# Kernel optimization log

Hardware: AMD Instinct MI355X
Metric: run time of the kernel (lower is better)

Reference implementation:

```python
import jax, jax.numpy as jnp
import numpy as np

N = 100000
E = 1600000
IN_C = 256
OUT_C = 128


def setup_inputs() -> dict:
    key = jax.random.key(0)
    ks = jax.random.split(key, 8)
    x = jax.random.normal(ks[0], (N, IN_C), dtype=jnp.float32)
    edge_index = jax.random.randint(ks[1], (2, E), 0, N, dtype=jnp.int64)
    # GCNConv params (weight + bias)
    W = jax.random.normal(ks[2], (IN_C, OUT_C), dtype=jnp.float32) / np.sqrt(IN_C)
    b = jnp.zeros((OUT_C,), dtype=jnp.float32)
    # residual Linear params
    Wr = jax.random.normal(ks[3], (IN_C, OUT_C), dtype=jnp.float32) / np.sqrt(IN_C)
    br = jnp.zeros((OUT_C,), dtype=jnp.float32)
    # LayerNorm params
    gamma = jnp.ones((OUT_C,), dtype=jnp.float32)
    beta = jnp.zeros((OUT_C,), dtype=jnp.float32)
    return {"x": x, "edge_index": edge_index, "W": W, "b": b,
            "Wr": Wr, "br": br, "gamma": gamma, "beta": beta}


def _gcn_conv(x, src, dst, W, b):
    # PyG GCNConv: add self-loops, symmetric degree normalization,
    # transform first (out < in), then gather-scale-scatter.
    n = x.shape[0]
    loops = jnp.arange(n, dtype=src.dtype)
    src = jnp.concatenate([src, loops])
    dst = jnp.concatenate([dst, loops])
    ones = jnp.ones_like(dst, dtype=x.dtype)
    deg = jax.ops.segment_sum(ones, dst, num_segments=n)  # [N]
    dinv = jnp.where(deg > 0, jax.lax.rsqrt(deg), 0.0)
    norm = dinv[src] * dinv[dst]                           # [E+N]
    h = x @ W                                              # [N, out]
    msg = h[src] * norm[:, None]                           # [E+N, out]
    agg = jax.ops.segment_sum(msg, dst, num_segments=n)    # [N, out]
    return agg + b


def _layer_norm(x, gamma, beta, eps=1e-5):
    mu = jnp.mean(x, axis=-1, keepdims=True)
    var = jnp.mean(jnp.square(x - mu), axis=-1, keepdims=True)
    return (x - mu) * jax.lax.rsqrt(var + eps) * gamma + beta


def reference(x, edge_index, W, b, Wr, br, gamma, beta):
    src, dst = edge_index[0], edge_index[1]
    res = x @ Wr + br
    h = _gcn_conv(x, src, dst, W, b)
    out = _layer_norm(h + res, gamma, beta)
    return jax.nn.relu(out)
```

## Files before the change

kernel.cpp:

```cpp
#include <hip/hip_runtime.h>

typedef __attribute__((ext_vector_type(8))) short bf16x8;
typedef __attribute__((ext_vector_type(4))) float f32x4;
typedef __attribute__((ext_vector_type(8))) unsigned short ushort8;
typedef __attribute__((ext_vector_type(4))) unsigned short ushort4v;

__device__ __forceinline__ unsigned short f2bf(float f) {
  unsigned int u = __float_as_uint(f);
  u = u + 0x7FFFu + ((u >> 16) & 1u);
  return (unsigned short)(u >> 16);
}
__device__ __forceinline__ float bflo(unsigned int u) { return __uint_as_float(u << 16); }
__device__ __forceinline__ float bfhi(unsigned int u) { return __uint_as_float(u & 0xFFFF0000u); }

#define GLOAD_LDS16(g, l)                                                            \
  __builtin_amdgcn_global_load_lds((const __attribute__((address_space(1))) void*)(g), \
                                   (__attribute__((address_space(3))) void*)(l), 16, 0, 0)

__global__ void k_pre(const float* __restrict__ W, const float* __restrict__ Wr,
                      unsigned short* __restrict__ Wb,
                      const int* __restrict__ dst, int* __restrict__ deg,
                      int* __restrict__ rank, int E) {
  if (blockIdx.x < 8) {
    int t = blockIdx.x * 256 + threadIdx.x;
    int col = t >> 3, g = t & 7;
    const float* Ws = (col < 128) ? (W + col) : (Wr + (col - 128));
#pragma unroll
    for (int kt = 0; kt < 4; ++kt) {
      ushort8 u;
#pragma unroll
      for (int j = 0; j < 8; ++j) u[j] = f2bf(Ws[(size_t)(kt * 64 + g * 8 + j) * 128]);
      *(ushort8*)&Wb[kt * 16384 + col * 64 + ((g ^ (col & 7)) * 8)] = u;
    }
    return;
  }
  int base = ((blockIdx.x - 8) * 256 + threadIdx.x) * 4;
  if (base + 3 < E) {
    int4 d = *(const int4*)(dst + base);
    int r0 = atomicAdd(&deg[d.x], 1);
    int r1 = atomicAdd(&deg[d.y], 1);
    int r2 = atomicAdd(&deg[d.z], 1);
    int r3 = atomicAdd(&deg[d.w], 1);
    *(int4*)(rank + base) = make_int4(r0, r1, r2, r3);
  } else {
    for (int e = base; e < E; ++e) rank[e] = atomicAdd(&deg[dst[e]], 1);
  }
}

__global__ void k_fill(const int* __restrict__ src, const int* __restrict__ dst,
                       const int* __restrict__ rank, int* __restrict__ ssrc, int E) {
  int base = (blockIdx.x * blockDim.x + threadIdx.x) * 4;
  if (base + 3 < E) {
    int4 d = *(const int4*)(dst + base);
    int4 r = *(const int4*)(rank + base);
    int4 s = *(const int4*)(src + base);
    if (r.x < 64) ssrc[(size_t)d.x * 64 + r.x] = s.x;
    if (r.y < 64) ssrc[(size_t)d.y * 64 + r.y] = s.y;
    if (r.z < 64) ssrc[(size_t)d.z * 64 + r.z] = s.z;
    if (r.w < 64) ssrc[(size_t)d.w * 64 + r.w] = s.w;
  } else {
    for (int e = base; e < E; ++e) {
      int r = rank[e];
      if (r < 64) ssrc[(size_t)dst[e] * 64 + r] = src[e];
    }
  }
}

__global__ __launch_bounds__(512) void k_gemm(
    const float* __restrict__ x, const unsigned short* __restrict__ Wb,
    const float* __restrict__ br, const int* __restrict__ deg,
    unsigned short* __restrict__ hs, float* res, int N)
{
  __shared__ unsigned short xt[128 * 64];
  __shared__ unsigned short wt[256 * 64];
  int tid = threadIdx.x;
  int lane = tid & 63, w = tid >> 6;
  int lo = lane & 15, hi = lane >> 4;
  int brow = blockIdx.x * 128;

  f32x4 acc[16];
#pragma unroll
  for (int c = 0; c < 16; ++c) acc[c] = (f32x4){0.f, 0.f, 0.f, 0.f};

  for (int kt = 0; kt < 4; ++kt) {
    int k0 = kt * 64;
    const unsigned short* gw = Wb + kt * 16384;
#pragma unroll
    for (int i = 0; i < 4; ++i) {
      int off = i * 4096 + tid * 8;
      GLOAD_LDS16(gw + off, &wt[off]);
    }
#pragma unroll
    for (int r = 0; r < 4; ++r) {
      int idx = tid + 512 * r;
      int row = idx >> 4, kq = idx & 15;
      int node = brow + row;
      float4 v = make_float4(0.f, 0.f, 0.f, 0.f);
      if (node < N) v = *(const float4*)(x + (size_t)node * 256 + k0 + kq * 4);
      ushort4v u;
      u[0] = f2bf(v.x); u[1] = f2bf(v.y); u[2] = f2bf(v.z); u[3] = f2bf(v.w);
      int g = kq >> 1, h = kq & 1;
      *(ushort4v*)(&xt[row * 64 + ((g ^ (row & 7)) * 8) + h * 4]) = u;
    }
    __syncthreads();
#pragma unroll
    for (int kk = 0; kk < 2; ++kk) {
      int row = w * 16 + lo;
      int gsel = kk * 4 + hi;
      bf16x8 a = *(const bf16x8*)(&xt[row * 64 + ((gsel ^ (row & 7)) * 8)]);
      int gsw = (gsel ^ (lo & 7)) * 8;
#pragma unroll
      for (int c = 0; c < 16; ++c) {
        bf16x8 b = *(const bf16x8*)(&wt[(c * 16 + lo) * 64 + gsw]);
        acc[c] = __builtin_amdgcn_mfma_f32_16x16x32_bf16(a, b, acc[c], 0, 0, 0);
      }
    }
    __syncthreads();
  }
  float di4[4];
#pragma unroll
  for (int rg = 0; rg < 4; ++rg) {
    int row = brow + w * 16 + hi * 4 + rg;
    di4[rg] = (row < N) ? rsqrtf((float)(deg[row] + 1)) : 0.f;
  }
#pragma unroll
  for (int c = 0; c < 16; ++c) {
    int colo = c * 16 + lo;
#pragma unroll
    for (int rg = 0; rg < 4; ++rg) {
      int row = brow + w * 16 + hi * 4 + rg;
      if (row < N) {
        float v = acc[c][rg];
        if (colo < 128) hs[(size_t)row * 128 + colo] = f2bf(v * di4[rg]);
        else            res[(size_t)row * 128 + (colo - 128)] = v + br[colo - 128];
      }
    }
  }
}

__global__ __launch_bounds__(256) void k_agg(
    const unsigned int* __restrict__ hsb, const float* resin,
    const int* __restrict__ deg, const int* __restrict__ ssrc,
    const float* __restrict__ bias, const float* __restrict__ gamma,
    const float* __restrict__ beta, float* out, int N)
{
  int node = blockIdx.x * 4 + (threadIdx.x >> 6);
  int lane = threadIdx.x & 63;
  if (node >= N) return;
  unsigned int su = hsb[(size_t)node * 64 + lane];
  float ax = bflo(su), ay = bfhi(su);
  int cnt = deg[node];
  float di = rsqrtf((float)(cnt + 1));
  if (cnt > 64) cnt = 64;
  const int* sp = ssrc + (size_t)node * 64;
  int e = 0;
  for (; e + 16 <= cnt; e += 16) {
    int idx[16];
#pragma unroll
    for (int j = 0; j < 16; ++j) idx[j] = sp[e + j];
    unsigned int u[16];
#pragma unroll
    for (int j = 0; j < 16; ++j) u[j] = hsb[(size_t)idx[j] * 64 + lane];
    float sx = 0.f, sy = 0.f;
#pragma unroll
    for (int j = 0; j < 16; ++j) { sx += bflo(u[j]); sy += bfhi(u[j]); }
    ax += sx; ay += sy;
  }
  for (; e + 4 <= cnt; e += 4) {
    int i0 = sp[e + 0], i1 = sp[e + 1], i2 = sp[e + 2], i3 = sp[e + 3];
    unsigned int u0 = hsb[(size_t)i0 * 64 + lane];
    unsigned int u1 = hsb[(size_t)i1 * 64 + lane];
    unsigned int u2 = hsb[(size_t)i2 * 64 + lane];
    unsigned int u3 = hsb[(size_t)i3 * 64 + lane];
    ax += (bflo(u0) + bflo(u1)) + (bflo(u2) + bflo(u3));
    ay += (bfhi(u0) + bfhi(u1)) + (bfhi(u2) + bfhi(u3));
  }
  for (; e < cnt; ++e) {
    int s = sp[e];
    unsigned int u = hsb[(size_t)s * 64 + lane];
    ax += bflo(u); ay += bfhi(u);
  }
  float2 r  = ((const float2*)resin)[(size_t)node * 64 + lane];
  float2 bb = ((const float2*)bias)[lane];
  float vx = ax * di + bb.x + r.x;
  float vy = ay * di + bb.y + r.y;
  float sum = vx + vy;
#pragma unroll
  for (int off = 32; off >= 1; off >>= 1) sum += __shfl_xor(sum, off, 64);
  float mean = sum * (1.0f / 128.0f);
  float dx = vx - mean, dy = vy - mean;
  float sq = dx * dx + dy * dy;
#pragma unroll
  for (int off = 32; off >= 1; off >>= 1) sq += __shfl_xor(sq, off, 64);
  float rstd = rsqrtf(sq * (1.0f / 128.0f) + 1e-5f);
  float2 g  = ((const float2*)gamma)[lane];
  float2 be = ((const float2*)beta)[lane];
  float ox = fmaxf(dx * rstd * g.x + be.x, 0.0f);
  float oy = fmaxf(dy * rstd * g.y + be.y, 0.0f);
  ((float2*)out)[(size_t)node * 64 + lane] = make_float2(ox, oy);
}

extern "C" void kernel_launch(void* const* d_in, const int* in_sizes, int n_in,
                              void* d_out, int out_size, void* d_ws, size_t ws_size,
                              hipStream_t stream) {
  const float* x     = (const float*)d_in[0];
  const int*   eidx  = (const int*)d_in[1];
  const float* W     = (const float*)d_in[2];
  const float* b     = (const float*)d_in[3];
  const float* Wr    = (const float*)d_in[4];
  const float* br    = (const float*)d_in[5];
  const float* gamma = (const float*)d_in[6];
  const float* beta  = (const float*)d_in[7];
  float* out = (float*)d_out;

  int N = in_sizes[0] / 256;
  int E = in_sizes[1] / 2;
  const int* srcI = eidx;
  const int* dstI = eidx + E;

  char* w = (char*)d_ws;
  size_t off = 0;
  auto alloc = [&](size_t bytes) -> void* {
    void* p = w + off;
    off += (bytes + 255) & ~(size_t)255;
    return p;
  };
  unsigned short* hs   = (unsigned short*)alloc((size_t)N * 128 * 2);
  int*   deg    = (int*)alloc((size_t)N * 4);
  int*   rank   = (int*)alloc((size_t)E * 4);
  int*   ssrc   = (int*)alloc((size_t)N * 64 * 4);
  unsigned short* Wb = (unsigned short*)alloc((size_t)4 * 16384 * 2);

  hipMemsetAsync(deg, 0, (size_t)N * 4, stream);
  int dgrid = (E / 4 + 255) / 256;
  k_pre <<<8 + dgrid, 256, 0, stream>>>(W, Wr, Wb, dstI, deg, rank, E);
  k_fill<<<dgrid, 256, 0, stream>>>(srcI, dstI, rank, ssrc, E);
  k_gemm<<<(N + 127) / 128, 512, 0, stream>>>(x, Wb, br, deg, hs, out, N);
  k_agg <<<(N + 3) / 4, 256, 0, stream>>>((const unsigned int*)hs, out, deg, ssrc,
                                          b, gamma, beta, out, N);
}
```

Measured before the change: 214.0 us.

## Split aggregation across two waves per node and precompute CSR slot indices

The degree pass now stores the final ssrc slot index, or -1 when the slot overflows, instead of the raw rank. The fill kernel then reads only src and slot and writes with nontemporal stores, skipping the dst reads. Each thread in both kernels now handles 8 edges. The aggregation kernel uses two waves per node, each covering half the channels, and each half-wave takes alternate neighbors, so one node gets twice the in-flight gathers. The cost is a cross-half shuffle, LDS exchange and two __syncthreads for the LayerNorm reductions, plus twice as many blocks.

Result: slower. 354.9 us (+65.9%).

```diff
diff --git a/kernel.cpp b/kernel.cpp
--- a/kernel.cpp
+++ b/kernel.cpp
@@ -20,7 +20,7 @@
 __global__ void k_pre(const float* __restrict__ W, const float* __restrict__ Wr,
                       unsigned short* __restrict__ Wb,
                       const int* __restrict__ dst, int* __restrict__ deg,
-                      int* __restrict__ rank, int E) {
+                      int* __restrict__ slot, int E) {
   if (blockIdx.x < 8) {
     int t = blockIdx.x * 256 + threadIdx.x;
     int col = t >> 3, g = t & 7;
@@ -34,34 +34,53 @@
     }
     return;
   }
-  int base = ((blockIdx.x - 8) * 256 + threadIdx.x) * 4;
-  if (base + 3 < E) {
-    int4 d = *(const int4*)(dst + base);
-    int r0 = atomicAdd(&deg[d.x], 1);
-    int r1 = atomicAdd(&deg[d.y], 1);
-    int r2 = atomicAdd(&deg[d.z], 1);
-    int r3 = atomicAdd(&deg[d.w], 1);
-    *(int4*)(rank + base) = make_int4(r0, r1, r2, r3);
-  } else {
-    for (int e = base; e < E; ++e) rank[e] = atomicAdd(&deg[dst[e]], 1);
-  }
-}
-
-__global__ void k_fill(const int* __restrict__ src, const int* __restrict__ dst,
-                       const int* __restrict__ rank, int* __restrict__ ssrc, int E) {
-  int base = (blockIdx.x * blockDim.x + threadIdx.x) * 4;
-  if (base + 3 < E) {
-    int4 d = *(const int4*)(dst + base);
-    int4 r = *(const int4*)(rank + base);
-    int4 s = *(const int4*)(src + base);
-    if (r.x < 64) ssrc[(size_t)d.x * 64 + r.x] = s.x;
-    if (r.y < 64) ssrc[(size_t)d.y * 64 + r.y] = s.y;
-    if (r.z < 64) ssrc[(size_t)d.z * 64 + r.z] = s.z;
-    if (r.w < 64) ssrc[(size_t)d.w * 64 + r.w] = s.w;
+  int base = ((blockIdx.x - 8) * 256 + threadIdx.x) * 8;
+  if (base + 7 < E) {
+    int4 d0 = *(const int4*)(dst + base);
+    int4 d1 = *(const int4*)(dst + base + 4);
+    int r0 = atomicAdd(&deg[d0.x], 1);
+    int r1 = atomicAdd(&deg[d0.y], 1);
+    int r2 = atomicAdd(&deg[d0.z], 1);
+    int r3 = atomicAdd(&deg[d0.w], 1);
+    int r4 = atomicAdd(&deg[d1.x], 1);
+    int r5 = atomicAdd(&deg[d1.y], 1);
+    int r6 = atomicAdd(&deg[d1.z], 1);
+    int r7 = atomicAdd(&deg[d1.w], 1);
+    int4 s0 = make_int4(r0 < 64 ? d0.x * 64 + r0 : -1, r1 < 64 ? d0.y * 64 + r1 : -1,
+                        r2 < 64 ? d0.z * 64 + r2 : -1, r3 < 64 ? d0.w * 64 + r3 : -1);
+    int4 s1 = make_int4(r4 < 64 ? d1.x * 64 + r4 : -1, r5 < 64 ? d1.y * 64 + r5 : -1,
+                        r6 < 64 ? d1.z * 64 + r6 : -1, r7 < 64 ? d1.w * 64 + r7 : -1);
+    *(int4*)(slot + base) = s0;
+    *(int4*)(slot + base + 4) = s1;
   } else {
     for (int e = base; e < E; ++e) {
-      int r = rank[e];
-      if (r < 64) ssrc[(size_t)dst[e] * 64 + r] = src[e];
+      int d = dst[e];
+      int r = atomicAdd(&deg[d], 1);
+      slot[e] = (r < 64) ? d * 64 + r : -1;
+    }
+  }
+}
+
+__global__ void k_fill(const int* __restrict__ src, const int* __restrict__ slot,
+                       int* __restrict__ ssrc, int E) {
+  int base = (blockIdx.x * blockDim.x + threadIdx.x) * 8;
+  if (base + 7 < E) {
+    int4 t0 = *(const int4*)(slot + base);
+    int4 t1 = *(const int4*)(slot + base + 4);
+    int4 s0 = *(const int4*)(src + base);
+    int4 s1 = *(const int4*)(src + base + 4);
+    if (t0.x >= 0) __builtin_nontemporal_store(s0.x, &ssrc[t0.x]);
+    if (t0.y >= 0) __builtin_nontemporal_store(s0.y, &ssrc[t0.y]);
+    if (t0.z >= 0) __builtin_nontemporal_store(s0.z, &ssrc[t0.z]);
+    if (t0.w >= 0) __builtin_nontemporal_store(s0.w, &ssrc[t0.w]);
+    if (t1.x >= 0) __builtin_nontemporal_store(s1.x, &ssrc[t1.x]);
+    if (t1.y >= 0) __builtin_nontemporal_store(s1.y, &ssrc[t1.y]);
+    if (t1.z >= 0) __builtin_nontemporal_store(s1.z, &ssrc[t1.z]);
+    if (t1.w >= 0) __builtin_nontemporal_store(s1.w, &ssrc[t1.w]);
+  } else {
+    for (int e = base; e < E; ++e) {
+      int t = slot[e];
+      if (t >= 0) __builtin_nontemporal_store(src[e], &ssrc[t]);
     }
   }
 }
@@ -144,60 +163,82 @@
     const float* __restrict__ bias, const float* __restrict__ gamma,
     const float* __restrict__ beta, float* out, int N)
 {
-  int node = blockIdx.x * 4 + (threadIdx.x >> 6);
+  __shared__ float pp[4], pq[4];
+  int wid = threadIdx.x >> 6;
   int lane = threadIdx.x & 63;
-  if (node >= N) return;
-  unsigned int su = hsb[(size_t)node * 64 + lane];
-  float ax = bflo(su), ay = bfhi(su);
+  int node = blockIdx.x * 2 + (wid >> 1);
+  if (node >= N) node = N - 1;
+  int half = wid & 1;
+  int hl = lane & 31, sel = lane >> 5;
+  int c = half * 32 + hl;
+
   int cnt = deg[node];
   float di = rsqrtf((float)(cnt + 1));
   if (cnt > 64) cnt = 64;
   const int* sp = ssrc + (size_t)node * 64;
+
+  float ax = 0.f, ay = 0.f;
+  if (sel == 0) {
+    unsigned int su = hsb[(size_t)node * 64 + c];
+    ax = bflo(su); ay = bfhi(su);
+  }
+
   int e = 0;
   for (; e + 16 <= cnt; e += 16) {
-    int idx[16];
-#pragma unroll
-    for (int j = 0; j < 16; ++j) idx[j] = sp[e + j];
-    unsigned int u[16];
-#pragma unroll
-    for (int j = 0; j < 16; ++j) u[j] = hsb[(size_t)idx[j] * 64 + lane];
+    int2 p[8];
+#pragma unroll
+    for (int j = 0; j < 8; ++j) p[j] = *(const int2*)(sp + e + 2 * j);
+    unsigned int u[8];
+#pragma unroll
+    for (int j = 0; j < 8; ++j) {
+      int row = sel ? p[j].y : p[j].x;
+      u[j] = hsb[(size_t)row * 64 + c];
+    }
     float sx = 0.f, sy = 0.f;
 #pragma unroll
-    for (int j = 0; j < 16; ++j) { sx += bflo(u[j]); sy += bfhi(u[j]); }
+    for (int j = 0; j < 8; ++j) { sx += bflo(u[j]); sy += bfhi(u[j]); }
     ax += sx; ay += sy;
   }
-  for (; e + 4 <= cnt; e += 4) {
-    int i0 = sp[e + 0], i1 = sp[e + 1], i2 = sp[e + 2], i3 = sp[e + 3];
-    unsigned int u0 = hsb[(size_t)i0 * 64 + lane];
-    unsigned int u1 = hsb[(size_t)i1 * 64 + lane];
-    unsigned int u2 = hsb[(size_t)i2 * 64 + lane];
-    unsigned int u3 = hsb[(size_t)i3 * 64 + lane];
-    ax += (bflo(u0) + bflo(u1)) + (bflo(u2) + bflo(u3));
-    ay += (bfhi(u0) + bfhi(u1)) + (bfhi(u2) + bfhi(u3));
-  }
-  for (; e < cnt; ++e) {
-    int s = sp[e];
-    unsigned int u = hsb[(size_t)s * 64 + lane];
+  for (; e + 2 <= cnt; e += 2) {
+    int2 p = *(const int2*)(sp + e);
+    int row = sel ? p.y : p.x;
+    unsigned int u = hsb[(size_t)row * 64 + c];
     ax += bflo(u); ay += bfhi(u);
   }
-  float2 r  = ((const float2*)resin)[(size_t)node * 64 + lane];
-  float2 bb = ((const float2*)bias)[lane];
-  float vx = ax * di + bb.x + r.x;
-  float vy = ay * di + bb.y + r.y;
-  float sum = vx + vy;
-#pragma unroll
-  for (int off = 32; off >= 1; off >>= 1) sum += __shfl_xor(sum, off, 64);
-  float mean = sum * (1.0f / 128.0f);
+  if (e < cnt && sel == 0) {
+    unsigned int u = hsb[(size_t)sp[e] * 64 + c];
+    ax += bflo(u); ay += bfhi(u);
+  }
+  ax += __shfl_xor(ax, 32, 64);
+  ay += __shfl_xor(ay, 32, 64);
+
+  float2 rr = ((const float2*)resin)[(size_t)node * 64 + c];
+  float2 bb = ((const float2*)bias)[c];
+  float vx = ax * di + bb.x + rr.x;
+  float vy = ay * di + bb.y + rr.y;
+
+  float s = vx + vy;
+#pragma unroll
+  for (int off = 1; off <= 16; off <<= 1) s += __shfl_xor(s, off, 64);
+  if (threadIdx.x == (unsigned)(wid * 64)) pp[wid] = s;
+  __syncthreads();
+  float mean = (pp[wid] + pp[wid ^ 1]) * (1.0f / 128.0f);
+
   float dx = vx - mean, dy = vy - mean;
   float sq = dx * dx + dy * dy;
 #pragma unroll
-  for (int off = 32; off >= 1; off >>= 1) sq += __shfl_xor(sq, off, 64);
-  float rstd = rsqrtf(sq * (1.0f / 128.0f) + 1e-5f);
-  float2 g  = ((const float2*)gamma)[lane];
-  float2 be = ((const float2*)beta)[lane];
-  float ox = fmaxf(dx * rstd * g.x + be.x, 0.0f);
-  float oy = fmaxf(dy * rstd * g.y + be.y, 0.0f);
-  ((float2*)out)[(size_t)node * 64 + lane] = make_float2(ox, oy);
+  for (int off = 1; off <= 16; off <<= 1) sq += __shfl_xor(sq, off, 64);
+  if (threadIdx.x == (unsigned)(wid * 64)) pq[wid] = sq;
+  __syncthreads();
+  float rstd = rsqrtf((pq[wid] + pq[wid ^ 1]) * (1.0f / 128.0f) + 1e-5f);
+
+  if (sel == 0) {
+    float2 g  = ((const float2*)gamma)[c];
+    float2 be = ((const float2*)beta)[c];
+    float ox = fmaxf(dx * rstd * g.x + be.x, 0.0f);
+    float oy = fmaxf(dy * rstd * g.y + be.y, 0.0f);
+    ((float2*)out)[(size_t)node * 64 + c] = make_float2(ox, oy);
+  }
 }
 
 extern "C" void kernel_launch(void* const* d_in, const int* in_sizes, int n_in,
@@ -227,15 +268,15 @@
   };
   unsigned short* hs   = (unsigned short*)alloc((size_t)N * 128 * 2);
   int*   deg    = (int*)alloc((size_t)N * 4);
-  int*   rank   = (int*)alloc((size_t)E * 4);
+  int*   slot   = (int*)alloc((size_t)E * 4);
   int*   ssrc   = (int*)alloc((size_t)N * 64 * 4);
   unsigned short* Wb = (unsigned short*)alloc((size_t)4 * 16384 * 2);
 
   hipMemsetAsync(deg, 0, (size_t)N * 4, stream);
-  int dgrid = (E / 4 + 255) / 256;
-  k_pre <<<8 + dgrid, 256, 0, stream>>>(W, Wr, Wb, dstI, deg, rank, E);
-  k_fill<<<dgrid, 256, 0, stream>>>(srcI, dstI, rank, ssrc, E);
+  int eg = (E + 2047) / 2048;
+  k_pre <<<8 + eg, 256, 0, stream>>>(W, Wr, Wb, dstI, deg, slot, E);
+  k_fill<<<eg, 256, 0, stream>>>(srcI, slot, ssrc, E);
   k_gemm<<<(N + 127) / 128, 512, 0, stream>>>(x, Wb, br, deg, hs, out, N);
-  k_agg <<<(N + 3) / 4, 256, 0, stream>>>((const unsigned int*)hs, out, deg, ssrc,
+  k_agg <<<(N + 1) / 2, 256, 0, stream>>>((const unsigned int*)hs, out, deg, ssrc,
                                           b, gamma, beta, out, N);
 }
```
